# Performance work log

Hardware: AMD Instinct MI355X
Metric: run time of the kernel (lower is better)

Reference implementation:

```python
import jax, jax.numpy as jnp
import numpy as np

B, T, C, H = 2, 2048, 1024, 16
D = C // H  # head dim = 64


def setup_inputs() -> dict:
    key = jax.random.key(0)
    k1, k2, k3 = jax.random.split(key, 3)
    x = jax.random.normal(k1, (B, T, C), dtype=jnp.float32)
    w_attn = jax.random.normal(k2, (C, 3 * C), dtype=jnp.float32) * (1.0 / np.sqrt(C))
    b_attn = jnp.zeros((3 * C,), dtype=jnp.float32)
    w_proj = jax.random.normal(k3, (C, C), dtype=jnp.float32) * (1.0 / np.sqrt(C))
    b_proj = jnp.zeros((C,), dtype=jnp.float32)
    return {"x": x, "w_attn": w_attn, "b_attn": b_attn, "w_proj": w_proj, "b_proj": b_proj}


def reference(x, w_attn, b_attn, w_proj, b_proj):
    Bx, Tx, Cx = x.shape
    qkv = x @ w_attn + b_attn  # [B, T, 3C]
    q, k, v = jnp.split(qkv, 3, axis=-1)
    # [B, H, T, D]
    q = q.reshape(Bx, Tx, H, D).swapaxes(1, 2)
    k = k.reshape(Bx, Tx, H, D).swapaxes(1, 2)
    v = v.reshape(Bx, Tx, H, D).swapaxes(1, 2)
    scale = 1.0 / jnp.sqrt(jnp.float32(D))
    att = jnp.einsum('bhqd,bhkd->bhqk', q, k) * scale  # [B, H, T, T]
    causal = jnp.tril(jnp.ones((Tx, Tx), dtype=bool))
    att = jnp.where(causal[None, None], att, -jnp.inf)
    att = jax.nn.softmax(att, axis=-1)
    y = jnp.einsum('bhqk,bhkd->bhqd', att, v)  # [B, H, T, D]
    y = y.swapaxes(1, 2).reshape(Bx, Tx, Cx)
    return y @ w_proj + b_proj
```

## Files before the change

### kernel.cpp

```cpp
#include <hip/hip_runtime.h>
#include <hip/hip_bf16.h>


typedef __attribute__((ext_vector_type(8))) short short8x;
typedef __attribute__((ext_vector_type(4))) float float4x;
typedef __attribute__((ext_vector_type(4))) unsigned short ushort4x;
typedef __attribute__((ext_vector_type(2))) unsigned int uint2x;

#define MFMA_BF16 __builtin_amdgcn_mfma_f32_16x16x32_bf16

typedef const __attribute__((address_space(1))) void gvoid_t;
typedef __attribute__((address_space(3))) void lvoid_t;
#define GLOAD_LDS16(g, l) __builtin_amdgcn_global_load_lds((gvoid_t*)(g), (lvoid_t*)(l), 16, 0, 0)

__device__ __forceinline__ unsigned short f2b(float f) {
    unsigned int u = __float_as_uint(f);
    u = (u + 0x7FFFu + ((u >> 16) & 1u)) >> 16;
    return (unsigned short)u;
}
__device__ __forceinline__ unsigned int pk2(float a, float b) {
    return __builtin_amdgcn_perm(__float_as_uint(b) + 0x8000u,
                                 __float_as_uint(a) + 0x8000u, 0x07060302u);
}

__device__ __forceinline__ void stage32(const unsigned short* g, size_t rs,
                                        short* ldst, int w0, int lane) {
    const int r8 = lane >> 3;
    const int sc = ((lane & 7) ^ r8) * 8;
#pragma unroll
    for (int q = 0; q < 4; q++) {
        GLOAD_LDS16(g + (size_t)(w0 + q * 8 + r8) * rs + sc,
                    ldst + (w0 + q * 8) * 64);
    }
}

__global__ __launch_bounds__(256) void cast_bf16(const float* __restrict__ in,
                                                 unsigned short* __restrict__ out,
                                                 int n4) {
    int i = blockIdx.x * 256 + threadIdx.x;
    if (i < n4) {
        float4 v = ((const float4*)in)[i];
        ushort4x o = { f2b(v.x), f2b(v.y), f2b(v.z), f2b(v.w) };
        ((ushort4x*)out)[i] = o;
    }
}

__global__ __launch_bounds__(256) void transpose_cast2(const float* __restrict__ wa,
                                                       unsigned short* __restrict__ waT,
                                                       const float* __restrict__ wp,
                                                       unsigned short* __restrict__ wpT) {
    __shared__ float tile[32][33];
    int bx = blockIdx.x;
    const float* in;
    unsigned short* outp;
    int cols;
    if (bx < 96) { in = wa; outp = waT; cols = 3072; }
    else         { in = wp; outp = wpT; cols = 1024; bx -= 96; }
    int cbase = bx * 32;
    int rbase = blockIdx.y * 32;
    int c = cbase + threadIdx.x;
    for (int j = 0; j < 32; j += 8)
        tile[threadIdx.y + j][threadIdx.x] = in[(size_t)(rbase + threadIdx.y + j) * cols + c];
    __syncthreads();
    int rr = rbase + threadIdx.x;
    for (int j = 0; j < 32; j += 8) {
        int cc = cbase + threadIdx.y + j;
        outp[(size_t)cc * 1024 + rr] = f2b(tile[threadIdx.x][threadIdx.y + j]);
    }
}

__global__ __launch_bounds__(256) void gemm_qkv(const unsigned short* __restrict__ A,
                                                const unsigned short* __restrict__ BT,
                                                const float* __restrict__ bias,
                                                unsigned short* __restrict__ QK,
                                                unsigned short* __restrict__ VTg) {
    __shared__ union {
        struct { short A[128 * 64]; short B[128 * 64]; } s;
        short vt[4][64 * 80];
    } lds;

    const int K = 1024;
    const int lane = threadIdx.x & 63;
    const int wave = threadIdx.x >> 6;
    const int quad = lane >> 4;
    const int l16  = lane & 15;
    const int sw   = l16 & 7;

    const int rblk = blockIdx.y * 128;
    const int cblk = blockIdx.x * 128;
    const int wr = wave >> 1, wc = wave & 1;

    float4x acc[4][4] = {};

    const unsigned short* Ag = A  + (size_t)rblk * K;
    const unsigned short* Bg = BT + (size_t)cblk * K;

    for (int kk = 0; kk < K; kk += 64) {
        stage32(Ag + kk, K, lds.s.A, wave * 32, lane);
        stage32(Bg + kk, K, lds.s.B, wave * 32, lane);
        __syncthreads();

#pragma unroll
        for (int kk2 = 0; kk2 < 2; kk2++) {
            short8x a[4], b[4];
#pragma unroll
            for (int i = 0; i < 4; i++)
                a[i] = *(const short8x*)&lds.s.A[(wr * 64 + i * 16 + l16) * 64 +
                                                 ((kk2 * 4 + quad) ^ sw) * 8];
#pragma unroll
            for (int j = 0; j < 4; j++)
                b[j] = *(const short8x*)&lds.s.B[(wc * 64 + j * 16 + l16) * 64 +
                                                 ((kk2 * 4 + quad) ^ sw) * 8];
#pragma unroll
            for (int i = 0; i < 4; i++)
#pragma unroll
                for (int j = 0; j < 4; j++)
                    acc[i][j] = MFMA_BF16(a[i], b[j], acc[i][j], 0, 0, 0);
        }
        __syncthreads();
    }

    const int rbase = rblk + wr * 64;
    const int cbase = cblk + wc * 64;

    if (cbase < 2048) {
        const float QS = 0.18033688f;
#pragma unroll
        for (int i = 0; i < 4; i++) {
#pragma unroll
            for (int j = 0; j < 4; j++) {
                int c = cbase + j * 16 + l16;
                float bv = bias[c];
                float sc = (c < 1024) ? QS : 1.0f;
#pragma unroll
                for (int reg = 0; reg < 4; reg++) {
                    int r = rbase + i * 16 + quad * 4 + reg;
                    QK[(size_t)r * 2048 + c] = f2b((acc[i][j][reg] + bv) * sc);
                }
            }
        }
    } else {
#pragma unroll
        for (int i = 0; i < 4; i++) {
#pragma unroll
            for (int j = 0; j < 4; j++) {
                int c = cbase + j * 16 + l16;
                float bv = bias[c];
                uint2x p = { pk2(acc[i][j][0] + bv, acc[i][j][1] + bv),
                             pk2(acc[i][j][2] + bv, acc[i][j][3] + bv) };
                *(uint2x*)&lds.vt[wave][(j * 16 + l16) * 80 + i * 16 + quad * 4] = p;
            }
        }
        const int h   = (cbase - 2048) >> 6;
        const int hb  = (rbase >> 11) * 16 + h;
        const int tb0 = rbase & 2047;
#pragma unroll
        for (int p = 0; p < 8; p++) {
            int dd   = p * 8 + (lane >> 3);
            int toff = (lane & 7) * 8;
            short8x vv = *(const short8x*)&lds.vt[wave][dd * 80 + toff];
            *(short8x*)&VTg[((size_t)(hb * 64 + dd)) * 2048 + tb0 + toff] = vv;
        }
    }
}

__global__ __launch_bounds__(256) void gemm_proj(const unsigned short* __restrict__ A,
                                                 const unsigned short* __restrict__ BT,
                                                 const float* __restrict__ bias,
                                                 float* __restrict__ out) {
    __shared__ struct { short A[64 * 64]; short B[64 * 64]; } lds;

    const int K = 1024, N = 1024;
    const int lane = threadIdx.x & 63;
    const int wave = threadIdx.x >> 6;
    const int quad = lane >> 4;
    const int l16  = lane & 15;
    const int sw   = l16 & 7;

    const int rblk = blockIdx.y * 64;
    const int cblk = blockIdx.x * 64;

    float4x acc[4] = {};

    const unsigned short* Ag = A  + (size_t)rblk * K;
    const unsigned short* Bg = BT + (size_t)cblk * K;

    for (int kk = 0; kk < K; kk += 64) {
        if (wave < 2) stage32(Ag + kk, K, lds.A, wave * 32, lane);
        else          stage32(Bg + kk, K, lds.B, (wave - 2) * 32, lane);
        __syncthreads();

#pragma unroll
        for (int kk2 = 0; kk2 < 2; kk2++) {
            short8x bfr = *(const short8x*)&lds.B[(wave * 16 + l16) * 64 +
                                                  ((kk2 * 4 + quad) ^ sw) * 8];
#pragma unroll
            for (int i = 0; i < 4; i++) {
                short8x a = *(const short8x*)&lds.A[(i * 16 + l16) * 64 +
                                                    ((kk2 * 4 + quad) ^ sw) * 8];
                acc[i] = MFMA_BF16(a, bfr, acc[i], 0, 0, 0);
            }
        }
        __syncthreads();
    }

    const int c = cblk + wave * 16 + l16;
    const float bv = bias[c];
#pragma unroll
    for (int i = 0; i < 4; i++) {
#pragma unroll
        for (int reg = 0; reg < 4; reg++) {
            int r = rblk + i * 16 + quad * 4 + reg;
            out[(size_t)r * N + c] = acc[i][reg] + bv;
        }
    }
}

__global__ __launch_bounds__(256) void attn_kernel(const unsigned short* __restrict__ QK,
                                                   const unsigned short* __restrict__ VT,
                                                   unsigned short* __restrict__ Y) {
    __shared__ __attribute__((aligned(16))) short Kl[2][64 * 64];
    __shared__ __attribute__((aligned(16))) short Vl[2][64 * 64];
    __shared__ __attribute__((aligned(16))) short Pl[4][16 * 64];

    const int tid  = threadIdx.x;
    const int lane = tid & 63;
    const int wave = tid >> 6;
    const int quad = lane >> 4;
    const int l16  = lane & 15;
    const int sw   = l16 & 7;

    const int level = blockIdx.x >> 5;
    const int bh    = blockIdx.x & 31;
    const int pair  = level >> 1;
    const int qb    = (level & 1) ? pair : (31 - pair);
    const int b = bh >> 4, h = bh & 15;

    const unsigned short* Qp = QK + ((size_t)b * 2048) * 2048 + h * 64;
    const unsigned short* Kp = Qp + 1024;
    const unsigned short* Vp = VT + (size_t)bh * 64 * 2048;

    const int qbase = qb * 64 + wave * 16;
    const int ntb   = qb + 1;

    short8x aq[2];
#pragma unroll
    for (int kk = 0; kk < 2; kk++)
        aq[kk] = *(const short8x*)(Qp + (size_t)(qbase + l16) * 2048 + kk * 32 + quad * 8);

    if (wave < 2) stage32(Kp, 2048, Kl[0], wave * 32, lane);
    else          stage32(Vp, 2048, Vl[0], (wave - 2) * 32, lane);
    __syncthreads();

    float l = 0.f;
    float4x O[4] = {};

    for (int it = 0; it < ntb; it++) {
        const int kb = it * 64;
        const short* Kc = Kl[it & 1];
        const short* Vc = Vl[it & 1];

        if (it + 1 < ntb) {
            const int kb2 = kb + 64;
            if (wave < 2) stage32(Kp + (size_t)kb2 * 2048, 2048, Kl[(it + 1) & 1], wave * 32, lane);
            else          stage32(Vp + kb2, 2048, Vl[(it + 1) & 1], (wave - 2) * 32, lane);
        }

        float4x S[4];
#pragma unroll
        for (int t = 0; t < 4; t++) {
            short8x kf0 = *(const short8x*)&Kc[(t * 16 + l16) * 64 + ((quad) ^ sw) * 8];
            short8x kf1 = *(const short8x*)&Kc[(t * 16 + l16) * 64 + ((4 + quad) ^ sw) * 8];
            S[t] = (float4x){0.f, 0.f, 0.f, 0.f};
            S[t] = MFMA_BF16(kf0, aq[0], S[t], 0, 0, 0);
            S[t] = MFMA_BF16(kf1, aq[1], S[t], 0, 0, 0);
        }

        if (kb + 64 > qbase) {
            int q = qbase + l16;
#pragma unroll
            for (int t = 0; t < 4; t++)
#pragma unroll
                for (int reg = 0; reg < 4; reg++)
                    if (kb + t * 16 + quad * 4 + reg > q) S[t][reg] = -1e38f;
        }

#pragma unroll
        for (int t = 0; t < 4; t++) {
            float e0 = __builtin_amdgcn_exp2f(S[t][0]);
            float e1 = __builtin_amdgcn_exp2f(S[t][1]);
            float e2 = __builtin_amdgcn_exp2f(S[t][2]);
            float e3 = __builtin_amdgcn_exp2f(S[t][3]);
            l += (e0 + e1) + (e2 + e3);
            uint2x p = { pk2(e0, e1), pk2(e2, e3) };
            *(uint2x*)&Pl[wave][l16 * 64 + ((2 * t + (quad >> 1)) ^ sw) * 8 + (quad & 1) * 4] = p;
        }

#pragma unroll
        for (int kc = 0; kc < 2; kc++) {
            short8x bp = *(const short8x*)&Pl[wave][l16 * 64 + ((4 * kc + quad) ^ sw) * 8];
#pragma unroll
            for (int dt = 0; dt < 4; dt++) {
                short8x vf = *(const short8x*)&Vc[(dt * 16 + l16) * 64 + ((kc * 4 + quad) ^ sw) * 8];
                O[dt] = MFMA_BF16(vf, bp, O[dt], 0, 0, 0);
            }
        }
        __syncthreads();
    }

    float lv = l;
    lv += __shfl_xor(lv, 16, 64);
    lv += __shfl_xor(lv, 32, 64);
    float rl = 1.0f / lv;
#pragma unroll
    for (int dt = 0; dt < 4; dt++) {
        uint2x o = { pk2(O[dt][0] * rl, O[dt][1] * rl),
                     pk2(O[dt][2] * rl, O[dt][3] * rl) };
        *(uint2x*)&Pl[wave][l16 * 64 + ((2 * dt + (quad >> 1)) ^ sw) * 8 + (quad & 1) * 4] = o;
    }
    const int t = qbase + l16;
#pragma unroll
    for (int cc = 0; cc < 2; cc++) {
        short8x row = *(const short8x*)&Pl[wave][l16 * 64 + ((2 * quad + cc) ^ sw) * 8];
        *(short8x*)&Y[((size_t)(b * 2048 + t)) * 1024 + h * 64 + (2 * quad + cc) * 8] = row;
    }
}

extern "C" void kernel_launch(void* const* d_in, const int* in_sizes, int n_in,
                              void* d_out, int out_size, void* d_ws, size_t ws_size,
                              hipStream_t stream) {
    const float* x      = (const float*)d_in[0];
    const float* w_attn = (const float*)d_in[1];
    const float* b_attn = (const float*)d_in[2];
    const float* w_proj = (const float*)d_in[3];
    const float* b_proj = (const float*)d_in[4];
    float* out = (float*)d_out;

    char* ws = (char*)d_ws;
    unsigned short* xb  = (unsigned short*)(ws + (size_t)0);
    unsigned short* waT = (unsigned short*)(ws + (size_t)(8  << 20));
    unsigned short* wpT = (unsigned short*)(ws + (size_t)(14 << 20));
    unsigned short* QKb = (unsigned short*)(ws + (size_t)(16 << 20));
    unsigned short* VTb = (unsigned short*)(ws + (size_t)(32 << 20));
    unsigned short* yb  = (unsigned short*)(ws + (size_t)(40 << 20));

    cast_bf16<<<4096, 256, 0, stream>>>(x, xb, 1048576);

    transpose_cast2<<<dim3(128, 32), dim3(32, 8), 0, stream>>>(w_attn, waT, w_proj, wpT);

    gemm_qkv<<<dim3(24, 32), 256, 0, stream>>>(xb, waT, b_attn, QKb, VTb);

    attn_kernel<<<1024, 256, 0, stream>>>(QKb, VTb, yb);

    gemm_proj<<<dim3(16, 64), 256, 0, stream>>>(yb, wpT, b_proj, out);
}
```

Baseline: 188.3 us.

## Halve attention KV tile, skip masked waves, MFMA row-sum, fuse prep kernels

The attention kernel now walks keys in 32-wide tiles, so each wave skips tiles that lie entirely beyond its causal limit, and each of the four waves issues one async load per tile. The softmax denominator is now computed with an MFMA against a ones vector on the bf16-rounded probabilities, replacing scalar adds and shuffles. LDS drops and launch bounds request 8 blocks per CU for more occupancy. The input cast and the weight transpose-cast are merged into one launch to save a kernel launch. The cost is twice as many loop iterations, each with a block-wide barrier.

```diff
diff --git a/kernel.cpp b/kernel.cpp
--- a/kernel.cpp
+++ b/kernel.cpp
@@ -34,38 +34,38 @@
     }
 }
 
-__global__ __launch_bounds__(256) void cast_bf16(const float* __restrict__ in,
-                                                 unsigned short* __restrict__ out,
-                                                 int n4) {
-    int i = blockIdx.x * 256 + threadIdx.x;
-    if (i < n4) {
-        float4 v = ((const float4*)in)[i];
+__global__ __launch_bounds__(256) void prep(const float* __restrict__ x,
+                                            unsigned short* __restrict__ xb,
+                                            const float* __restrict__ wa,
+                                            unsigned short* __restrict__ waT,
+                                            const float* __restrict__ wp,
+                                            unsigned short* __restrict__ wpT) {
+    __shared__ float tile[32][33];
+    const int bid = blockIdx.x;
+    const int tid = threadIdx.x;
+    if (bid < 4096) {
+        int i = bid * 256 + tid;
+        float4 v = ((const float4*)x)[i];
         ushort4x o = { f2b(v.x), f2b(v.y), f2b(v.z), f2b(v.w) };
-        ((ushort4x*)out)[i] = o;
-    }
-}
-
-__global__ __launch_bounds__(256) void transpose_cast2(const float* __restrict__ wa,
-                                                       unsigned short* __restrict__ waT,
-                                                       const float* __restrict__ wp,
-                                                       unsigned short* __restrict__ wpT) {
-    __shared__ float tile[32][33];
-    int bx = blockIdx.x;
+        ((ushort4x*)xb)[i] = o;
+        return;
+    }
+    int b2 = bid - 4096;
     const float* in;
     unsigned short* outp;
-    int cols;
-    if (bx < 96) { in = wa; outp = waT; cols = 3072; }
-    else         { in = wp; outp = wpT; cols = 1024; bx -= 96; }
-    int cbase = bx * 32;
-    int rbase = blockIdx.y * 32;
-    int c = cbase + threadIdx.x;
+    int cols, bx, by;
+    if (b2 < 3072) { in = wa; outp = waT; cols = 3072; bx = b2 % 96; by = b2 / 96; }
+    else { b2 -= 3072; in = wp; outp = wpT; cols = 1024; bx = b2 & 31; by = b2 >> 5; }
+    const int tx = tid & 31, ty = tid >> 5;
+    const int cbase = bx * 32, rbase = by * 32;
+    const int c = cbase + tx;
     for (int j = 0; j < 32; j += 8)
-        tile[threadIdx.y + j][threadIdx.x] = in[(size_t)(rbase + threadIdx.y + j) * cols + c];
+        tile[ty + j][tx] = in[(size_t)(rbase + ty + j) * cols + c];
     __syncthreads();
-    int rr = rbase + threadIdx.x;
+    const int rr = rbase + tx;
     for (int j = 0; j < 32; j += 8) {
-        int cc = cbase + threadIdx.y + j;
-        outp[(size_t)cc * 1024 + rr] = f2b(tile[threadIdx.x][threadIdx.y + j]);
+        int cc = cbase + ty + j;
+        outp[(size_t)cc * 1024 + rr] = f2b(tile[tx][ty + j]);
     }
 }
 
@@ -216,19 +216,20 @@
     }
 }
 
-__global__ __launch_bounds__(256) void attn_kernel(const unsigned short* __restrict__ QK,
-                                                   const unsigned short* __restrict__ VT,
-                                                   unsigned short* __restrict__ Y) {
-    __shared__ __attribute__((aligned(16))) short Kl[2][64 * 64];
-    __shared__ __attribute__((aligned(16))) short Vl[2][64 * 64];
-    __shared__ __attribute__((aligned(16))) short Pl[4][16 * 64];
+__global__ __launch_bounds__(256, 8) void attn_kernel(const unsigned short* __restrict__ QK,
+                                                      const unsigned short* __restrict__ VT,
+                                                      unsigned short* __restrict__ Y) {
+    __shared__ __attribute__((aligned(16))) short Kl[2][32 * 64];
+    __shared__ __attribute__((aligned(16))) short Vl[2][64 * 32];
+    __shared__ __attribute__((aligned(16))) short Pl[4][16 * 32];
 
     const int tid  = threadIdx.x;
     const int lane = tid & 63;
     const int wave = tid >> 6;
     const int quad = lane >> 4;
     const int l16  = lane & 15;
-    const int sw   = l16 & 7;
+    const int sw3  = l16 & 3;
+    const int sw7  = l16 & 7;
 
     const int level = blockIdx.x >> 5;
     const int bh    = blockIdx.x & 31;
@@ -241,87 +242,93 @@
     const unsigned short* Vp = VT + (size_t)bh * 64 * 2048;
 
     const int qbase = qb * 64 + wave * 16;
-    const int ntb   = qb + 1;
+    const int kend  = qbase + 16;
+    const int ntb   = 2 * qb + 2;
 
     short8x aq[2];
 #pragma unroll
     for (int kk = 0; kk < 2; kk++)
         aq[kk] = *(const short8x*)(Qp + (size_t)(qbase + l16) * 2048 + kk * 32 + quad * 8);
 
-    if (wave < 2) stage32(Kp, 2048, Kl[0], wave * 32, lane);
-    else          stage32(Vp, 2048, Vl[0], (wave - 2) * 32, lane);
+    short8x ones;
+#pragma unroll
+    for (int e = 0; e < 8; e++) ones[e] = (short)0x3F80;
+
+    const int krow = wave * 8 + (lane >> 3);
+    const unsigned short* Kg = Kp + (size_t)krow * 2048 + ((lane & 7) ^ (lane >> 3)) * 8;
+    const int vrow = wave * 16 + (lane >> 2);
+    const unsigned short* Vg = Vp + (size_t)vrow * 2048 + (((lane & 3) ^ ((lane >> 2) & 3)) * 8);
+
+    GLOAD_LDS16(Kg, &Kl[0][wave * 8 * 64]);
+    GLOAD_LDS16(Vg, &Vl[0][wave * 16 * 32]);
     __syncthreads();
 
-    float l = 0.f;
     float4x O[4] = {};
+    float4x lacc = {};
 
     for (int it = 0; it < ntb; it++) {
-        const int kb = it * 64;
+        const int kb = it * 32;
         const short* Kc = Kl[it & 1];
         const short* Vc = Vl[it & 1];
 
         if (it + 1 < ntb) {
-            const int kb2 = kb + 64;
-            if (wave < 2) stage32(Kp + (size_t)kb2 * 2048, 2048, Kl[(it + 1) & 1], wave * 32, lane);
-            else          stage32(Vp + kb2, 2048, Vl[(it + 1) & 1], (wave - 2) * 32, lane);
-        }
-
-        float4x S[4];
-#pragma unroll
-        for (int t = 0; t < 4; t++) {
-            short8x kf0 = *(const short8x*)&Kc[(t * 16 + l16) * 64 + ((quad) ^ sw) * 8];
-            short8x kf1 = *(const short8x*)&Kc[(t * 16 + l16) * 64 + ((4 + quad) ^ sw) * 8];
-            S[t] = (float4x){0.f, 0.f, 0.f, 0.f};
-            S[t] = MFMA_BF16(kf0, aq[0], S[t], 0, 0, 0);
-            S[t] = MFMA_BF16(kf1, aq[1], S[t], 0, 0, 0);
-        }
-
-        if (kb + 64 > qbase) {
-            int q = qbase + l16;
-#pragma unroll
-            for (int t = 0; t < 4; t++)
-#pragma unroll
-                for (int reg = 0; reg < 4; reg++)
-                    if (kb + t * 16 + quad * 4 + reg > q) S[t][reg] = -1e38f;
-        }
-
-#pragma unroll
-        for (int t = 0; t < 4; t++) {
-            float e0 = __builtin_amdgcn_exp2f(S[t][0]);
-            float e1 = __builtin_amdgcn_exp2f(S[t][1]);
-            float e2 = __builtin_amdgcn_exp2f(S[t][2]);
-            float e3 = __builtin_amdgcn_exp2f(S[t][3]);
-            l += (e0 + e1) + (e2 + e3);
-            uint2x p = { pk2(e0, e1), pk2(e2, e3) };
-            *(uint2x*)&Pl[wave][l16 * 64 + ((2 * t + (quad >> 1)) ^ sw) * 8 + (quad & 1) * 4] = p;
-        }
-
-#pragma unroll
-        for (int kc = 0; kc < 2; kc++) {
-            short8x bp = *(const short8x*)&Pl[wave][l16 * 64 + ((4 * kc + quad) ^ sw) * 8];
+            GLOAD_LDS16(Kg + (size_t)(kb + 32) * 2048, &Kl[(it + 1) & 1][wave * 8 * 64]);
+            GLOAD_LDS16(Vg + (kb + 32), &Vl[(it + 1) & 1][wave * 16 * 32]);
+        }
+
+        if (kb < kend) {
+            float4x S[2];
+#pragma unroll
+            for (int t = 0; t < 2; t++) {
+                short8x kf0 = *(const short8x*)&Kc[(t * 16 + l16) * 64 + ((quad) ^ sw7) * 8];
+                short8x kf1 = *(const short8x*)&Kc[(t * 16 + l16) * 64 + ((4 + quad) ^ sw7) * 8];
+                S[t] = (float4x){0.f, 0.f, 0.f, 0.f};
+                S[t] = MFMA_BF16(kf0, aq[0], S[t], 0, 0, 0);
+                S[t] = MFMA_BF16(kf1, aq[1], S[t], 0, 0, 0);
+            }
+
+            if (kb + 32 > qbase) {
+                int q = qbase + l16;
+#pragma unroll
+                for (int t = 0; t < 2; t++)
+#pragma unroll
+                    for (int reg = 0; reg < 4; reg++)
+                        if (kb + t * 16 + quad * 4 + reg > q) S[t][reg] = -1e38f;
+            }
+
+#pragma unroll
+            for (int t = 0; t < 2; t++) {
+                float e0 = __builtin_amdgcn_exp2f(S[t][0]);
+                float e1 = __builtin_amdgcn_exp2f(S[t][1]);
+                float e2 = __builtin_amdgcn_exp2f(S[t][2]);
+                float e3 = __builtin_amdgcn_exp2f(S[t][3]);
+                uint2x p = { pk2(e0, e1), pk2(e2, e3) };
+                *(uint2x*)&Pl[wave][l16 * 32 + ((t * 2 + (quad >> 1)) ^ sw3) * 8 + (quad & 1) * 4] = p;
+            }
+
+            short8x bp = *(const short8x*)&Pl[wave][l16 * 32 + (quad ^ sw3) * 8];
+            lacc = MFMA_BF16(ones, bp, lacc, 0, 0, 0);
 #pragma unroll
             for (int dt = 0; dt < 4; dt++) {
-                short8x vf = *(const short8x*)&Vc[(dt * 16 + l16) * 64 + ((kc * 4 + quad) ^ sw) * 8];
+                short8x vf = *(const short8x*)&Vc[(dt * 16 + l16) * 32 + (quad ^ sw3) * 8];
                 O[dt] = MFMA_BF16(vf, bp, O[dt], 0, 0, 0);
             }
         }
         __syncthreads();
     }
 
-    float lv = l;
-    lv += __shfl_xor(lv, 16, 64);
-    lv += __shfl_xor(lv, 32, 64);
-    float rl = 1.0f / lv;
+    float rl = 1.0f / lacc[0];
+    short* scr = &Kl[0][0] + wave * 1024;
 #pragma unroll
     for (int dt = 0; dt < 4; dt++) {
         uint2x o = { pk2(O[dt][0] * rl, O[dt][1] * rl),
                      pk2(O[dt][2] * rl, O[dt][3] * rl) };
-        *(uint2x*)&Pl[wave][l16 * 64 + ((2 * dt + (quad >> 1)) ^ sw) * 8 + (quad & 1) * 4] = o;
+        *(uint2x*)&scr[l16 * 64 + ((2 * dt + (quad >> 1)) ^ sw7) * 8 + (quad & 1) * 4] = o;
     }
     const int t = qbase + l16;
 #pragma unroll
     for (int cc = 0; cc < 2; cc++) {
-        short8x row = *(const short8x*)&Pl[wave][l16 * 64 + ((2 * quad + cc) ^ sw) * 8];
+        short8x row = *(const short8x*)&scr[l16 * 64 + ((2 * quad + cc) ^ sw7) * 8];
         *(short8x*)&Y[((size_t)(b * 2048 + t)) * 1024 + h * 64 + (2 * quad + cc) * 8] = row;
     }
 }
@@ -344,9 +351,7 @@
     unsigned short* VTb = (unsigned short*)(ws + (size_t)(32 << 20));
     unsigned short* yb  = (unsigned short*)(ws + (size_t)(40 << 20));
 
-    cast_bf16<<<4096, 256, 0, stream>>>(x, xb, 1048576);
-
-    transpose_cast2<<<dim3(128, 32), dim3(32, 8), 0, stream>>>(w_attn, waT, w_proj, wpT);
+    prep<<<8192, 256, 0, stream>>>(x, xb, w_attn, waT, w_proj, wpT);
 
     gemm_qkv<<<dim3(24, 32), 256, 0, stream>>>(xb, waT, b_attn, QKb, VTb);
 
```

New measurement: 200.1 us. 6.3% more time.
